# Performance work log

Hardware: AMD Instinct MI355X
Metric: run time of the kernel (lower is better)

## Reference

```python
import jax, jax.numpy as jnp
import numpy as np

P = 4; PSIZE = 16; EPS = 1e-8; LAM = 1e-3; MF = 2.0; ITERS = 2
BATCH = 64; A = 64; B = 8; C = 16; D = 16; E = 10


def _conv2d(x, w, b, stride, pad):
    y = jax.lax.conv_general_dilated(x, w, (stride, stride), [(pad, pad), (pad, pad)],
                                     dimension_numbers=('NCHW', 'OIHW', 'NCHW'))
    return y + b[None, :, None, None]


def _patches(x, K, stride):
    # x: (b, H, W, F) -> (b, oh, ow, K, K, F) sliding KxK windows with given stride
    b, H, W, F = x.shape
    oh = (H - K) // stride + 1
    ow = (W - K) // stride + 1
    ih = jnp.arange(oh) * stride
    iw = jnp.arange(ow) * stride
    p = x[:, ih[:, None] + jnp.arange(K)[None, :]]          # (b, oh, K, W, F)
    p = p[:, :, :, iw[:, None] + jnp.arange(K)[None, :]]    # (b, oh, K, ow, K, F)
    return p.transpose(0, 1, 3, 2, 4, 5), oh, ow


def _fuzzy_routing(v, a_in, beta_u, beta_a):
    # Fuzzy (c-means style) routing. v: (n, N, Cout, PSIZE) votes, a_in: (n, N).
    n, N, Cc, _ = v.shape
    r = jnp.full((n, N, Cc), 1.0 / Cc, dtype=v.dtype)
    aw = a_in[:, :, None]
    for t in range(ITERS):
        rm = (r ** MF) * aw                                             # fuzzified, activation-weighted
        coeff = rm / (jnp.sum(rm, axis=1, keepdims=True) + EPS)         # (n, N, C)
        mu = jnp.einsum('bnc,bncp->bcp', coeff, v)                      # (n, C, PSIZE)
        if t < ITERS - 1:
            dist = jnp.sum((v - mu[:, None]) ** 2, axis=-1) + EPS       # (n, N, C)
            inv = dist ** (-1.0 / (MF - 1.0))
            r = inv / (jnp.sum(inv, axis=2, keepdims=True) + EPS)
    sigma_sq = jnp.einsum('bnc,bncp->bcp', coeff, (v - mu[:, None]) ** 2) + EPS
    r_sum = jnp.sum((r ** MF) * aw, axis=1)                             # (n, C)
    cost = (beta_u[None, :, None] + 0.5 * jnp.log(sigma_sq)) * r_sum[:, :, None]
    a_out = jax.nn.sigmoid(LAM * (beta_a[None, :] - jnp.sum(cost, axis=2)))
    return mu, a_out


def _conv_caps(pose, a, W, beta_u, beta_a, K, stride):
    # pose: (b, H, W, Bi, PSIZE), a: (b, H, W, Bi); W: (K*K*Bi, Co, P, P)
    b, H, Wd, Bi, _ = pose.shape
    Co = W.shape[1]
    pp, oh, ow = _patches(pose.reshape(b, H, Wd, Bi * PSIZE), K, stride)
    ap, _, _ = _patches(a, K, stride)
    n = b * oh * ow
    pp = pp.reshape(n, K * K * Bi, P, P)
    ap = ap.reshape(n, K * K * Bi)
    v = jnp.einsum('nipq,icqr->nicpr', pp, W).reshape(n, K * K * Bi, Co, PSIZE)
    mu, a_out = _fuzzy_routing(v, ap, beta_u, beta_a)
    return mu.reshape(b, oh, ow, Co, PSIZE), a_out.reshape(b, oh, ow, Co)


def _class_caps(pose, a, W, beta_u, beta_a):
    # K=1, weight-shared over positions, with coordinate addition.
    b, H, Wd, Bi, _ = pose.shape
    Co = W.shape[1]
    v = jnp.einsum('bhwipq,icqr->bhwicpr', pose.reshape(b, H, Wd, Bi, P, P), W)
    v = v.reshape(b, H, Wd, Bi, Co, PSIZE)
    ch = (jnp.arange(H, dtype=v.dtype) / H)[None, :, None, None, None]
    cw = (jnp.arange(Wd, dtype=v.dtype) / Wd)[None, None, :, None, None]
    v = v.at[..., 0].add(ch)
    v = v.at[..., 1].add(cw)
    v = v.reshape(b, H * Wd * Bi, Co, PSIZE)
    return _fuzzy_routing(v, a.reshape(b, -1), beta_u, beta_a)


def setup_inputs():
    key = jax.random.key(0)
    ks = jax.random.split(key, 8)
    return {
        'x': jax.random.normal(ks[0], (BATCH, 1, 32, 32), jnp.float32),
        'conv1_w': jax.random.normal(ks[1], (A, 1, 5, 5), jnp.float32) * 0.1,
        'conv1_b': jnp.zeros((A,), jnp.float32),
        'bn_g': jnp.ones((A,), jnp.float32),
        'bn_b': jnp.zeros((A,), jnp.float32),
        'bn_mean': jnp.zeros((A,), jnp.float32),
        'bn_var': jnp.ones((A,), jnp.float32),
        'prim_pose_w': jax.random.normal(ks[2], (B * PSIZE, A, 1, 1), jnp.float32) * 0.1,
        'prim_pose_b': jnp.zeros((B * PSIZE,), jnp.float32),
        'prim_a_w': jax.random.normal(ks[3], (B, A, 1, 1), jnp.float32) * 0.1,
        'prim_a_b': jnp.zeros((B,), jnp.float32),
        'w1': jax.random.normal(ks[4], (3 * 3 * B, C, P, P), jnp.float32),
        'bu1': jnp.zeros((C,), jnp.float32),
        'ba1': jnp.zeros((C,), jnp.float32),
        'w2': jax.random.normal(ks[5], (3 * 3 * C, D, P, P), jnp.float32),
        'bu2': jnp.zeros((D,), jnp.float32),
        'ba2': jnp.zeros((D,), jnp.float32),
        'wc': jax.random.normal(ks[6], (D, E, P, P), jnp.float32),
        'buc': jnp.zeros((E,), jnp.float32),
        'bac': jnp.zeros((E,), jnp.float32),
    }


def reference(x, conv1_w, conv1_b, bn_g, bn_b, bn_mean, bn_var,
              prim_pose_w, prim_pose_b, prim_a_w, prim_a_b,
              w1, bu1, ba1, w2, bu2, ba2, wc, buc, bac):
    y = _conv2d(x, conv1_w, conv1_b, 2, 2)                               # (b, A, 16, 16)
    inv_std = jax.lax.rsqrt(bn_var + 1e-3)
    y = (y - bn_mean[None, :, None, None]) * (bn_g * inv_std)[None, :, None, None] + bn_b[None, :, None, None]
    y = jax.nn.relu(y)
    pose = _conv2d(y, prim_pose_w, prim_pose_b, 1, 0)                    # (b, B*16, 16, 16)
    a = jax.nn.sigmoid(_conv2d(y, prim_a_w, prim_a_b, 1, 0))             # (b, B, 16, 16)
    b_, _, H, Wd = a.shape
    pose = pose.transpose(0, 2, 3, 1).reshape(b_, H, Wd, B, PSIZE)
    a = a.transpose(0, 2, 3, 1)
    pose1, a1 = _conv_caps(pose, a, w1, bu1, ba1, 3, 2)
    pose2, a2 = _conv_caps(pose1, a1, w2, bu2, ba2, 3, 1)
    _, a_class = _class_caps(pose2, a2, wc, buc, bac)                    # (b, E)
    return a_class
```

## Files before the change

### kernel.cpp

```cpp
#include <hip/hip_runtime.h>
#include <math.h>

#define EPS_ 1e-8f
#define LAM_ 1e-3f

__global__ __launch_bounds__(256) void k_conv_bn(
    const float* __restrict__ x, const float* __restrict__ cw, const float* __restrict__ cb,
    const float* __restrict__ g, const float* __restrict__ bb,
    const float* __restrict__ mean, const float* __restrict__ var,
    float* __restrict__ y)
{
    int t = blockIdx.x * 256 + threadIdx.x;
    int ch = t & 63, w = (t >> 6) & 15, h = (t >> 10) & 15, b = t >> 14;
    const float* xb = x + b * 1024;
    const float* wc = cw + ch * 25;
    float acc = cb[ch];
    #pragma unroll
    for (int kh = 0; kh < 5; ++kh) {
        int ih = h * 2 - 2 + kh;
        if (ih < 0 || ih > 31) continue;
        #pragma unroll
        for (int kw = 0; kw < 5; ++kw) {
            int iw = w * 2 - 2 + kw;
            if (iw < 0 || iw > 31) continue;
            acc = fmaf(xb[ih * 32 + iw], wc[kh * 5 + kw], acc);
        }
    }
    float v = (acc - mean[ch]) * (g[ch] * rsqrtf(var[ch] + 1e-3f)) + bb[ch];
    y[t] = fmaxf(v, 0.f);
}

__global__ __launch_bounds__(256) void k_transw(
    const float* __restrict__ w1, const float* __restrict__ w2, const float* __restrict__ wc,
    const float* __restrict__ pw, const float* __restrict__ pb,
    const float* __restrict__ aw, const float* __restrict__ ab,
    float* __restrict__ w1t, float* __restrict__ w2t, float* __restrict__ wct,
    float* __restrict__ wpt)
{
    int t = blockIdx.x * 256 + threadIdx.x;
    if (t < 3616 * 16) {
        int m = t >> 4, e = t & 15, r = e >> 2, q = e & 3;
        const float* src; float* dst;
        if (m < 1152)      { src = w1 + m * 16;          dst = w1t + m * 16; }
        else if (m < 3456) { src = w2 + (m - 1152) * 16; dst = w2t + (m - 1152) * 16; }
        else               { src = wc + (m - 3456) * 16; dst = wct + (m - 3456) * 16; }
        dst[e] = src[q * 4 + r];
    } else if (t < 3616 * 16 + 65 * 136) {
        int idx = t - 3616 * 16;
        int o = idx % 136, j = idx / 136;
        float v;
        if (j == 64)       v = (o < 128) ? pb[o] : ab[o - 128];
        else if (o < 128)  v = pw[o * 64 + j];
        else               v = aw[(o - 128) * 64 + j];
        wpt[j * 136 + o] = v;
    }
}

__global__ __launch_bounds__(256) void k_prim(
    const float* __restrict__ y, const float* __restrict__ wpt,
    float* __restrict__ poseP, float* __restrict__ aP)
{
    int t = blockIdx.x * 256 + threadIdx.x;
    if (t >= 16384 * 34) return;
    int oq = t % 34;
    int pos = t / 34;
    const float* yp = y + pos * 64;
    float4 acc = *(const float4*)(wpt + 64 * 136 + oq * 4);
    #pragma unroll
    for (int j0 = 0; j0 < 64; j0 += 4) {
        float4 y4 = *(const float4*)(yp + j0);
        float4 w0 = *(const float4*)(wpt + (j0 + 0) * 136 + oq * 4);
        float4 w1 = *(const float4*)(wpt + (j0 + 1) * 136 + oq * 4);
        float4 w2 = *(const float4*)(wpt + (j0 + 2) * 136 + oq * 4);
        float4 w3 = *(const float4*)(wpt + (j0 + 3) * 136 + oq * 4);
        acc.x = fmaf(y4.x, w0.x, fmaf(y4.y, w1.x, fmaf(y4.z, w2.x, fmaf(y4.w, w3.x, acc.x))));
        acc.y = fmaf(y4.x, w0.y, fmaf(y4.y, w1.y, fmaf(y4.z, w2.y, fmaf(y4.w, w3.y, acc.y))));
        acc.z = fmaf(y4.x, w0.z, fmaf(y4.y, w1.z, fmaf(y4.z, w2.z, fmaf(y4.w, w3.z, acc.z))));
        acc.w = fmaf(y4.x, w0.w, fmaf(y4.y, w1.w, fmaf(y4.z, w2.w, fmaf(y4.w, w3.w, acc.w))));
    }
    if (oq < 32) {
        ((float4*)(poseP + pos * 128))[oq] = acc;
    } else {
        int oo = (oq - 32) * 4;
        float* ad = aP + pos * 8 + oo;
        ad[0] = 1.f / (1.f + expf(-acc.x));
        ad[1] = 1.f / (1.f + expf(-acc.y));
        ad[2] = 1.f / (1.f + expf(-acc.z));
        ad[3] = 1.f / (1.f + expf(-acc.w));
    }
}

template<int N, int C, int K, int S, int H, int W, int Bi, int OH, int OW, bool COORDS, int BLK>
__global__ __launch_bounds__(BLK) void k_caps(
    const float* __restrict__ pose_in,
    const float* __restrict__ a_in,
    const float* __restrict__ Wt,
    const float* __restrict__ bu, const float* __restrict__ ba,
    float* __restrict__ pose_out,
    float* __restrict__ a_out)
{
    constexpr int NW  = BLK / 64;
    constexpr int NIG = BLK / 16;
    constexpr int NIT = (N + NIG - 1) / NIG;

    __shared__ __align__(16) float pp[N * 16];
    __shared__ float ap[N];
    __shared__ float coeff0[N];
    __shared__ float mu0[16 * 17];
    __shared__ float red1[NW * C * 17];
    __shared__ float red2[NW * C * 17];
    __shared__ float redr[NW * C];

    const int t = threadIdx.x;
    const int lane = t & 63;
    const int w = t >> 6;
    const int n_ = blockIdx.x;
    const int b = n_ / (OH * OW);
    const int rem = n_ % (OH * OW);
    const int oh = rem / OW, ow = rem % OW;

    for (int idx = t; idx < N * 4; idx += BLK) {
        int i = idx >> 2, f = idx & 3;
        int bi = i % Bi;
        int sh, sw;
        if constexpr (COORDS) { int hw = i / Bi; sw = hw % W; sh = hw / W; }
        else { int k2 = i / Bi; sw = ow * S + (k2 % K); sh = oh * S + (k2 / K); }
        const float4* src = (const float4*)(pose_in + (((b * H + sh) * W + sw) * Bi + bi) * 16);
        ((float4*)(pp + i * 16))[f] = src[f];
    }
    for (int i = t; i < N; i += BLK) {
        int bi = i % Bi;
        int sh, sw;
        if constexpr (COORDS) { int hw = i / Bi; sw = hw % W; sh = hw / W; }
        else { int k2 = i / Bi; sw = ow * S + (k2 % K); sh = oh * S + (k2 / K); }
        ap[i] = a_in[((b * H + sh) * W + sw) * Bi + bi];
    }
    __syncthreads();

    {
        float part = 0.f;
        for (int i = t; i < N; i += BLK) part += ap[i];
        #pragma unroll
        for (int m = 1; m < 64; m <<= 1) part += __shfl_xor(part, m, 64);
        if (lane == 0) red1[w] = part;
        __syncthreads();
        float s = 0.f;
        #pragma unroll
        for (int ww = 0; ww < NW; ++ww) s += red1[ww];
        float inv0 = 1.f / (s + (float)(C * C) * EPS_);
        for (int i = t; i < N; i += BLK) coeff0[i] = ap[i] * inv0;
        __syncthreads();
    }

    const int ig = t >> 4, cc = t & 15;

    {
        float muU[16];
        #pragma unroll
        for (int e2 = 0; e2 < 16; ++e2) muU[e2] = 0.f;
        if (cc < C) {
            for (int ii = 0; ii < NIT; ++ii) {
                int i = ig + ii * NIG;
                if (i < N) {
                    const float4* pi4 = (const float4*)(pp + i * 16);
                    int widx = COORDS ? (i % Bi) : i;
                    const float4* wt4 = (const float4*)(Wt + (widx * C + cc) * 16);
                    float4 pv[4] = { pi4[0], pi4[1], pi4[2], pi4[3] };
                    float4 wv[4] = { wt4[0], wt4[1], wt4[2], wt4[3] };
                    float co = coeff0[i];
                    float chv = 0.f, cwv = 0.f;
                    if constexpr (COORDS) {
                        chv = (float)(i / (W * Bi)) * (1.f / H);
                        cwv = (float)((i / Bi) % W) * (1.f / W);
                    }
                    #pragma unroll
                    for (int e2 = 0; e2 < 16; ++e2) {
                        float4 p4 = pv[e2 >> 2], w4 = wv[e2 & 3];
                        float v = p4.x * w4.x + p4.y * w4.y + p4.z * w4.z + p4.w * w4.w;
                        if constexpr (COORDS) { if (e2 == 0) v += chv; if (e2 == 1) v += cwv; }
                        muU[e2] = fmaf(co, v, muU[e2]);
                    }
                }
            }
        }
        #pragma unroll
        for (int e2 = 0; e2 < 16; ++e2) {
            float xv = muU[e2];
            xv += __shfl_xor(xv, 16, 64);
            xv += __shfl_xor(xv, 32, 64);
            if (lane < 16 && lane < C) red1[(w * C + lane) * 17 + e2] = xv;
        }
        __syncthreads();
        if (t < 256) {
            int c = t >> 4, e = t & 15;
            if (c < C) {
                float m = 0.f;
                #pragma unroll
                for (int ww = 0; ww < NW; ++ww) m += red1[(ww * C + c) * 17 + e];
                mu0[c * 17 + e] = m;
            }
        }
        __syncthreads();
    }

    {
        float m0[16];
        if (cc < C) {
            #pragma unroll
            for (int e2 = 0; e2 < 16; ++e2) m0[e2] = mu0[cc * 17 + e2];
        }
        float SvU[16], Sv2U[16];
        #pragma unroll
        for (int e2 = 0; e2 < 16; ++e2) { SvU[e2] = 0.f; Sv2U[e2] = 0.f; }
        float rsumP = 0.f;

        for (int ii = 0; ii < NIT; ++ii) {
            int i = ig + ii * NIG;
            bool act = (i < N);
            float inv = 0.f;
            float vv[16];
            if (act && cc < C) {
                const float4* pi4 = (const float4*)(pp + i * 16);
                int widx = COORDS ? (i % Bi) : i;
                const float4* wt4 = (const float4*)(Wt + (widx * C + cc) * 16);
                float4 pv[4] = { pi4[0], pi4[1], pi4[2], pi4[3] };
                float4 wv[4] = { wt4[0], wt4[1], wt4[2], wt4[3] };
                float chv = 0.f, cwv = 0.f;
                if constexpr (COORDS) {
                    chv = (float)(i / (W * Bi)) * (1.f / H);
                    cwv = (float)((i / Bi) % W) * (1.f / W);
                }
                float dist = EPS_;
                #pragma unroll
                for (int e2 = 0; e2 < 16; ++e2) {
                    float4 p4 = pv[e2 >> 2], w4 = wv[e2 & 3];
                    float v = p4.x * w4.x + p4.y * w4.y + p4.z * w4.z + p4.w * w4.w;
                    if constexpr (COORDS) { if (e2 == 0) v += chv; if (e2 == 1) v += cwv; }
                    vv[e2] = v;
                    float d = v - m0[e2];
                    dist = fmaf(d, d, dist);
                }
                inv = 1.f / dist;
            }
            float s = inv;
            #pragma unroll
            for (int m = 1; m < 16; m <<= 1) s += __shfl_xor(s, m, 64);
            if (act && cc < C) {
                float r1 = inv / (s + EPS_);
                float rm = r1 * r1 * ap[i];
                rsumP += rm;
                #pragma unroll
                for (int e2 = 0; e2 < 16; ++e2) {
                    SvU[e2] = fmaf(rm, vv[e2], SvU[e2]);
                    Sv2U[e2] = fmaf(rm * vv[e2], vv[e2], Sv2U[e2]);
                }
            }
        }
        #pragma unroll
        for (int e2 = 0; e2 < 16; ++e2) {
            float xv = SvU[e2];
            xv += __shfl_xor(xv, 16, 64);
            xv += __shfl_xor(xv, 32, 64);
            float yv = Sv2U[e2];
            yv += __shfl_xor(yv, 16, 64);
            yv += __shfl_xor(yv, 32, 64);
            if (lane < 16 && lane < C) {
                red1[(w * C + lane) * 17 + e2] = xv;
                red2[(w * C + lane) * 17 + e2] = yv;
            }
        }
        {
            float rv = rsumP;
            rv += __shfl_xor(rv, 16, 64);
            rv += __shfl_xor(rv, 32, 64);
            if (lane < 16 && lane < C) redr[w * C + lane] = rv;
        }
        __syncthreads();
    }

    if (t < 256) {
        int c = t >> 4, e = t & 15;
        if (c < C) {
            float SvT = 0.f, Sv2T = 0.f, R = 0.f;
            #pragma unroll
            for (int ww = 0; ww < NW; ++ww) {
                SvT  += red1[(ww * C + c) * 17 + e];
                Sv2T += red2[(ww * C + c) * 17 + e];
                R    += redr[ww * C + c];
            }
            float id = 1.f / (R + EPS_);
            float S0 = R * id;
            float Sv = SvT * id;
            float Sv2 = Sv2T * id;
            float sigma = fmaxf(Sv2 + Sv * Sv * (S0 - 2.f), 0.f) + EPS_;
            float cost = (bu[c] + 0.5f * logf(sigma)) * R;
            float cs = cost;
            #pragma unroll
            for (int m = 1; m < 16; m <<= 1) cs += __shfl_xor(cs, m, 64);
            if constexpr (!COORDS) {
                pose_out[(n_ * C + c) * 16 + e] = Sv;
                if (e == 0) a_out[n_ * C + c] = 1.f / (1.f + expf(-(LAM_ * (ba[c] - cs))));
            } else {
                if (e == 0) a_out[b * C + c] = 1.f / (1.f + expf(-(LAM_ * (ba[c] - cs))));
            }
        }
    }
}

extern "C" void kernel_launch(void* const* d_in, const int* in_sizes, int n_in,
                              void* d_out, int out_size, void* d_ws, size_t ws_size,
                              hipStream_t stream)
{
    const float* x   = (const float*)d_in[0];
    const float* c1w = (const float*)d_in[1];
    const float* c1b = (const float*)d_in[2];
    const float* bng = (const float*)d_in[3];
    const float* bnb = (const float*)d_in[4];
    const float* bnm = (const float*)d_in[5];
    const float* bnv = (const float*)d_in[6];
    const float* ppw = (const float*)d_in[7];
    const float* ppb = (const float*)d_in[8];
    const float* paw = (const float*)d_in[9];
    const float* pab = (const float*)d_in[10];
    const float* w1  = (const float*)d_in[11];
    const float* bu1 = (const float*)d_in[12];
    const float* ba1 = (const float*)d_in[13];
    const float* w2  = (const float*)d_in[14];
    const float* bu2 = (const float*)d_in[15];
    const float* ba2 = (const float*)d_in[16];
    const float* wcp = (const float*)d_in[17];
    const float* buc = (const float*)d_in[18];
    const float* bac = (const float*)d_in[19];
    float* out = (float*)d_out;

    float* ws    = (float*)d_ws;
    float* y     = ws;
    float* poseP = y + 1048576;
    float* aP    = poseP + 2097152;
    float* pose1 = aP + 131072;
    float* a1    = pose1 + 802816;
    float* pose2 = a1 + 50176;
    float* a2    = pose2 + 409600;
    float* w1t   = a2 + 25600;
    float* w2t   = w1t + 18432;
    float* wct   = w2t + 36864;
    float* wpt   = wct + 2560;

    hipLaunchKernelGGL(k_transw, dim3((3616 * 16 + 65 * 136 + 255) / 256), dim3(256), 0, stream,
                       w1, w2, wcp, ppw, ppb, paw, pab, w1t, w2t, wct, wpt);
    hipLaunchKernelGGL(k_conv_bn, dim3(4096), dim3(256), 0, stream,
                       x, c1w, c1b, bng, bnb, bnm, bnv, y);
    hipLaunchKernelGGL(k_prim, dim3((16384 * 34 + 255) / 256), dim3(256), 0, stream,
                       y, wpt, poseP, aP);
    hipLaunchKernelGGL((k_caps<72, 16, 3, 2, 16, 16, 8, 7, 7, false, 256>), dim3(64 * 7 * 7), dim3(256), 0, stream,
                       poseP, aP, w1t, bu1, ba1, pose1, a1);
    hipLaunchKernelGGL((k_caps<144, 16, 3, 1, 7, 7, 16, 5, 5, false, 256>), dim3(64 * 5 * 5), dim3(256), 0, stream,
                       pose1, a1, w2t, bu2, ba2, pose2, a2);
    hipLaunchKernelGGL((k_caps<400, 10, 1, 1, 5, 5, 16, 1, 1, true, 1024>), dim3(64), dim3(1024), 0, stream,
                       pose2, a2, wct, buc, bac, nullptr, out);
}
```

Before: 280.9 us.

## Process each conv-capsule position with a single wavefront instead of a 256-thread block

Adds a k_caps_wave kernel that assigns one 64-lane wavefront per output capsule position, packing two positions into each 128-thread block. All reductions become wave shuffles instead of shared-memory staging with __syncthreads. It also uses fast intrinsics (rcp, __expf, __logf) for the sigmoid and routing math. The class-capsule path is split into its own kernel without the COORDS template. The aim is to remove barrier and shared-memory reduction overhead and idle threads, at the cost of each lane looping over more input capsules and slightly lower-precision math.

```diff
diff --git a/kernel.cpp b/kernel.cpp
--- a/kernel.cpp
+++ b/kernel.cpp
@@ -83,20 +83,156 @@
     } else {
         int oo = (oq - 32) * 4;
         float* ad = aP + pos * 8 + oo;
-        ad[0] = 1.f / (1.f + expf(-acc.x));
-        ad[1] = 1.f / (1.f + expf(-acc.y));
-        ad[2] = 1.f / (1.f + expf(-acc.z));
-        ad[3] = 1.f / (1.f + expf(-acc.w));
-    }
-}
-
-template<int N, int C, int K, int S, int H, int W, int Bi, int OH, int OW, bool COORDS, int BLK>
-__global__ __launch_bounds__(BLK) void k_caps(
+        ad[0] = 1.f / (1.f + __expf(-acc.x));
+        ad[1] = 1.f / (1.f + __expf(-acc.y));
+        ad[2] = 1.f / (1.f + __expf(-acc.z));
+        ad[3] = 1.f / (1.f + __expf(-acc.w));
+    }
+}
+
+template<int N, int C, int K, int S, int H, int W, int Bi, int OH, int OW>
+__global__ __launch_bounds__(128) void k_caps_wave(
     const float* __restrict__ pose_in,
     const float* __restrict__ a_in,
     const float* __restrict__ Wt,
     const float* __restrict__ bu, const float* __restrict__ ba,
     float* __restrict__ pose_out,
+    float* __restrict__ a_out)
+{
+    static_assert(C == 16 && N % 4 == 0, "");
+    constexpr int NIT = N / 4;
+
+    __shared__ __align__(16) float pp[2 * N * 16];
+    __shared__ float ap[2 * N];
+
+    const int t = threadIdx.x;
+    const int w = t >> 6, lane = t & 63;
+    float* ppw = pp + w * N * 16;
+    float* apw = ap + w * N;
+
+    const int n_ = blockIdx.x * 2 + w;
+    const int b = n_ / (OH * OW);
+    const int rem = n_ % (OH * OW);
+    const int oh = rem / OW, ow = rem % OW;
+
+    for (int idx = lane; idx < N * 4; idx += 64) {
+        int i = idx >> 2, f = idx & 3;
+        int bi = i % Bi;
+        int k2 = i / Bi;
+        int sw = ow * S + (k2 % K), sh = oh * S + (k2 / K);
+        const float4* src = (const float4*)(pose_in + (((b * H + sh) * W + sw) * Bi + bi) * 16);
+        ((float4*)(ppw + i * 16))[f] = src[f];
+    }
+    for (int i = lane; i < N; i += 64) {
+        int bi = i % Bi;
+        int k2 = i / Bi;
+        int sw = ow * S + (k2 % K), sh = oh * S + (k2 / K);
+        apw[i] = a_in[((b * H + sh) * W + sw) * Bi + bi];
+    }
+    __syncthreads();
+
+    float suma = 0.f;
+    for (int i = lane; i < N; i += 64) suma += apw[i];
+    #pragma unroll
+    for (int m = 1; m < 64; m <<= 1) suma += __shfl_xor(suma, m, 64);
+    const float inv0 = __builtin_amdgcn_rcpf(suma + (float)(C * C) * EPS_);
+
+    const int ig = t >> 4 & 3, cc = t & 15;
+
+    float muU[16];
+    #pragma unroll
+    for (int e2 = 0; e2 < 16; ++e2) muU[e2] = 0.f;
+    #pragma unroll 2
+    for (int ii = 0; ii < NIT; ++ii) {
+        int i = ig + ii * 4;
+        const float4* pi4 = (const float4*)(ppw + i * 16);
+        const float4* wt4 = (const float4*)(Wt + (i * C + cc) * 16);
+        float4 pv[4] = { pi4[0], pi4[1], pi4[2], pi4[3] };
+        float4 wv[4] = { wt4[0], wt4[1], wt4[2], wt4[3] };
+        float co = apw[i] * inv0;
+        #pragma unroll
+        for (int e2 = 0; e2 < 16; ++e2) {
+            float4 p4 = pv[e2 >> 2], w4 = wv[e2 & 3];
+            float v = p4.x * w4.x + p4.y * w4.y + p4.z * w4.z + p4.w * w4.w;
+            muU[e2] = fmaf(co, v, muU[e2]);
+        }
+    }
+    #pragma unroll
+    for (int e2 = 0; e2 < 16; ++e2) {
+        muU[e2] += __shfl_xor(muU[e2], 16, 64);
+        muU[e2] += __shfl_xor(muU[e2], 32, 64);
+    }
+
+    float SvU[16], Sv2U[16];
+    #pragma unroll
+    for (int e2 = 0; e2 < 16; ++e2) { SvU[e2] = 0.f; Sv2U[e2] = 0.f; }
+    float rsum = 0.f;
+    #pragma unroll 2
+    for (int ii = 0; ii < NIT; ++ii) {
+        int i = ig + ii * 4;
+        const float4* pi4 = (const float4*)(ppw + i * 16);
+        const float4* wt4 = (const float4*)(Wt + (i * C + cc) * 16);
+        float4 pv[4] = { pi4[0], pi4[1], pi4[2], pi4[3] };
+        float4 wv[4] = { wt4[0], wt4[1], wt4[2], wt4[3] };
+        float vv[16];
+        float dist = EPS_;
+        #pragma unroll
+        for (int e2 = 0; e2 < 16; ++e2) {
+            float4 p4 = pv[e2 >> 2], w4 = wv[e2 & 3];
+            float v = p4.x * w4.x + p4.y * w4.y + p4.z * w4.z + p4.w * w4.w;
+            vv[e2] = v;
+            float d = v - muU[e2];
+            dist = fmaf(d, d, dist);
+        }
+        float inv = __builtin_amdgcn_rcpf(dist);
+        float s = inv;
+        #pragma unroll
+        for (int m = 1; m < 16; m <<= 1) s += __shfl_xor(s, m, 64);
+        float r1 = inv * __builtin_amdgcn_rcpf(s + EPS_);
+        float rm = r1 * r1 * apw[i];
+        rsum += rm;
+        #pragma unroll
+        for (int e2 = 0; e2 < 16; ++e2) {
+            float rv = rm * vv[e2];
+            SvU[e2] += rv;
+            Sv2U[e2] = fmaf(rv, vv[e2], Sv2U[e2]);
+        }
+    }
+    #pragma unroll
+    for (int e2 = 0; e2 < 16; ++e2) {
+        SvU[e2] += __shfl_xor(SvU[e2], 16, 64);
+        SvU[e2] += __shfl_xor(SvU[e2], 32, 64);
+        Sv2U[e2] += __shfl_xor(Sv2U[e2], 16, 64);
+        Sv2U[e2] += __shfl_xor(Sv2U[e2], 32, 64);
+    }
+    rsum += __shfl_xor(rsum, 16, 64);
+    rsum += __shfl_xor(rsum, 32, 64);
+
+    const float id = 1.f / (rsum + EPS_);
+    const float S0 = rsum * id;
+    const float buc_ = bu[cc];
+    float cs = 0.f;
+    float4 outv[4];
+    #pragma unroll
+    for (int e2 = 0; e2 < 16; ++e2) {
+        float Sv = SvU[e2] * id;
+        float Sv2 = Sv2U[e2] * id;
+        float sigma = fmaxf(Sv2 + Sv * Sv * (S0 - 2.f), 0.f) + EPS_;
+        cs += (buc_ + 0.5f * __logf(sigma)) * rsum;
+        ((float*)outv)[e2] = Sv;
+    }
+    if (lane < 16) {
+        float4* pd = (float4*)(pose_out + (n_ * C + cc) * 16);
+        pd[0] = outv[0]; pd[1] = outv[1]; pd[2] = outv[2]; pd[3] = outv[3];
+        a_out[n_ * C + cc] = 1.f / (1.f + __expf(-(LAM_ * (ba[cc] - cs))));
+    }
+}
+
+template<int N, int C, int H, int W, int Bi, int BLK>
+__global__ __launch_bounds__(BLK) void k_caps_class(
+    const float* __restrict__ pose_in, const float* __restrict__ a_in,
+    const float* __restrict__ Wt,
+    const float* __restrict__ bu, const float* __restrict__ ba,
     float* __restrict__ a_out)
 {
     constexpr int NW  = BLK / 64;
@@ -114,25 +250,20 @@
     const int t = threadIdx.x;
     const int lane = t & 63;
     const int w = t >> 6;
-    const int n_ = blockIdx.x;
-    const int b = n_ / (OH * OW);
-    const int rem = n_ % (OH * OW);
-    const int oh = rem / OW, ow = rem % OW;
+    const int b = blockIdx.x;
 
     for (int idx = t; idx < N * 4; idx += BLK) {
         int i = idx >> 2, f = idx & 3;
         int bi = i % Bi;
-        int sh, sw;
-        if constexpr (COORDS) { int hw = i / Bi; sw = hw % W; sh = hw / W; }
-        else { int k2 = i / Bi; sw = ow * S + (k2 % K); sh = oh * S + (k2 / K); }
+        int hw = i / Bi;
+        int sw = hw % W, sh = hw / W;
         const float4* src = (const float4*)(pose_in + (((b * H + sh) * W + sw) * Bi + bi) * 16);
         ((float4*)(pp + i * 16))[f] = src[f];
     }
     for (int i = t; i < N; i += BLK) {
         int bi = i % Bi;
-        int sh, sw;
-        if constexpr (COORDS) { int hw = i / Bi; sw = hw % W; sh = hw / W; }
-        else { int k2 = i / Bi; sw = ow * S + (k2 % K); sh = oh * S + (k2 / K); }
+        int hw = i / Bi;
+        int sw = hw % W, sh = hw / W;
         ap[i] = a_in[((b * H + sh) * W + sw) * Bi + bi];
     }
     __syncthreads();
@@ -163,21 +294,18 @@
                 int i = ig + ii * NIG;
                 if (i < N) {
                     const float4* pi4 = (const float4*)(pp + i * 16);
-                    int widx = COORDS ? (i % Bi) : i;
-                    const float4* wt4 = (const float4*)(Wt + (widx * C + cc) * 16);
+                    const float4* wt4 = (const float4*)(Wt + ((i % Bi) * C + cc) * 16);
                     float4 pv[4] = { pi4[0], pi4[1], pi4[2], pi4[3] };
                     float4 wv[4] = { wt4[0], wt4[1], wt4[2], wt4[3] };
                     float co = coeff0[i];
-                    float chv = 0.f, cwv = 0.f;
-                    if constexpr (COORDS) {
-                        chv = (float)(i / (W * Bi)) * (1.f / H);
-                        cwv = (float)((i / Bi) % W) * (1.f / W);
-                    }
+                    float chv = (float)(i / (W * Bi)) * (1.f / H);
+                    float cwv = (float)((i / Bi) % W) * (1.f / W);
                     #pragma unroll
                     for (int e2 = 0; e2 < 16; ++e2) {
                         float4 p4 = pv[e2 >> 2], w4 = wv[e2 & 3];
                         float v = p4.x * w4.x + p4.y * w4.y + p4.z * w4.z + p4.w * w4.w;
-                        if constexpr (COORDS) { if (e2 == 0) v += chv; if (e2 == 1) v += cwv; }
+                        if (e2 == 0) v += chv;
+                        if (e2 == 1) v += cwv;
                         muU[e2] = fmaf(co, v, muU[e2]);
                     }
                 }
@@ -221,21 +349,18 @@
             float vv[16];
             if (act && cc < C) {
                 const float4* pi4 = (const float4*)(pp + i * 16);
-                int widx = COORDS ? (i % Bi) : i;
-                const float4* wt4 = (const float4*)(Wt + (widx * C + cc) * 16);
+                const float4* wt4 = (const float4*)(Wt + ((i % Bi) * C + cc) * 16);
                 float4 pv[4] = { pi4[0], pi4[1], pi4[2], pi4[3] };
                 float4 wv[4] = { wt4[0], wt4[1], wt4[2], wt4[3] };
-                float chv = 0.f, cwv = 0.f;
-                if constexpr (COORDS) {
-                    chv = (float)(i / (W * Bi)) * (1.f / H);
-                    cwv = (float)((i / Bi) % W) * (1.f / W);
-                }
+                float chv = (float)(i / (W * Bi)) * (1.f / H);
+                float cwv = (float)((i / Bi) % W) * (1.f / W);
                 float dist = EPS_;
                 #pragma unroll
                 for (int e2 = 0; e2 < 16; ++e2) {
                     float4 p4 = pv[e2 >> 2], w4 = wv[e2 & 3];
                     float v = p4.x * w4.x + p4.y * w4.y + p4.z * w4.z + p4.w * w4.w;
-                    if constexpr (COORDS) { if (e2 == 0) v += chv; if (e2 == 1) v += cwv; }
+                    if (e2 == 0) v += chv;
+                    if (e2 == 1) v += cwv;
                     vv[e2] = v;
                     float d = v - m0[e2];
                     dist = fmaf(d, d, dist);
@@ -297,12 +422,7 @@
             float cs = cost;
             #pragma unroll
             for (int m = 1; m < 16; m <<= 1) cs += __shfl_xor(cs, m, 64);
-            if constexpr (!COORDS) {
-                pose_out[(n_ * C + c) * 16 + e] = Sv;
-                if (e == 0) a_out[n_ * C + c] = 1.f / (1.f + expf(-(LAM_ * (ba[c] - cs))));
-            } else {
-                if (e == 0) a_out[b * C + c] = 1.f / (1.f + expf(-(LAM_ * (ba[c] - cs))));
-            }
+            if (e == 0) a_out[b * C + c] = 1.f / (1.f + expf(-(LAM_ * (ba[c] - cs))));
         }
     }
 }
@@ -352,10 +472,10 @@
                        x, c1w, c1b, bng, bnb, bnm, bnv, y);
     hipLaunchKernelGGL(k_prim, dim3((16384 * 34 + 255) / 256), dim3(256), 0, stream,
                        y, wpt, poseP, aP);
-    hipLaunchKernelGGL((k_caps<72, 16, 3, 2, 16, 16, 8, 7, 7, false, 256>), dim3(64 * 7 * 7), dim3(256), 0, stream,
+    hipLaunchKernelGGL((k_caps_wave<72, 16, 3, 2, 16, 16, 8, 7, 7>), dim3(1568), dim3(128), 0, stream,
                        poseP, aP, w1t, bu1, ba1, pose1, a1);
-    hipLaunchKernelGGL((k_caps<144, 16, 3, 1, 7, 7, 16, 5, 5, false, 256>), dim3(64 * 5 * 5), dim3(256), 0, stream,
+    hipLaunchKernelGGL((k_caps_wave<144, 16, 3, 1, 7, 7, 16, 5, 5>), dim3(800), dim3(128), 0, stream,
                        pose1, a1, w2t, bu2, ba2, pose2, a2);
-    hipLaunchKernelGGL((k_caps<400, 10, 1, 1, 5, 5, 16, 1, 1, true, 1024>), dim3(64), dim3(1024), 0, stream,
-                       pose2, a2, wct, buc, bac, nullptr, out);
-}
+    hipLaunchKernelGGL((k_caps_class<400, 10, 5, 5, 16, 1024>), dim3(64), dim3(1024), 0, stream,
+                       pose2, a2, wct, buc, bac, out);
+}
```

Measured after the change: 253.8 us. 9.7% less time.
